# Optimization experiments

Measured on AMD Instinct MI355X. Metric: run time of the kernel, lower is better.

The kernel has to match this reference:

```python
import jax, jax.numpy as jnp
import numpy as np
import math

D = 2048      # hidden_size
H = 16        # num_heads
DH = 128      # head_dim
RQ = 1024     # q_rank
RK = 512      # kv_rank
B, T = 2, 2048

def setup_inputs() -> dict:
    key = jax.random.key(0)
    ks = jax.random.split(key, 8)
    s = lambda fan_in: 1.0 / math.sqrt(fan_in)
    return {
        "x": jax.random.normal(ks[0], (B, T, D), dtype=jnp.float32),
        "Wq_down": jax.random.normal(ks[1], (RQ, D), dtype=jnp.float32) * s(D),
        "Wkv_down": jax.random.normal(ks[2], (RK, D), dtype=jnp.float32) * s(D),
        "Wq_up": jax.random.normal(ks[3], (D, RQ), dtype=jnp.float32) * s(RQ),
        "Wk_up": jax.random.normal(ks[4], (D, RK), dtype=jnp.float32) * s(RK),
        "Wv_up": jax.random.normal(ks[5], (D, RK), dtype=jnp.float32) * s(RK),
        "Wo": jax.random.normal(ks[6], (D, D), dtype=jnp.float32) * s(D),
        "bo": jnp.zeros((D,), dtype=jnp.float32),
    }

def _heads_view(w, rank):
    # w: [H*DH, rank] -> [H, rank, DH]  (matches torch view(H,DH,r).transpose(1,2))
    return w.reshape(H, DH, rank).transpose(0, 2, 1)

def reference(x, Wq_down, Wkv_down, Wq_up, Wk_up, Wv_up, Wo, bo):
    Bx, Tx, d = x.shape
    # low-rank down-projections (torch Linear: x @ W.T)
    Q_lat = x @ Wq_down.T            # [B,T,RQ]
    C_kv = x @ Wkv_down.T            # [B,S,RK]  (S == T, no cache)
    S = C_kv.shape[1]
    # absorbed score matrix M = Uq Uk^T / sqrt(d_h): [H,RQ,RK]
    Uq_h = _heads_view(Wq_up, RQ)    # [H,RQ,DH]
    Uk_h = _heads_view(Wk_up, RK)    # [H,RK,DH]
    Mmat = jnp.einsum('hqd,hkd->hqk', Uq_h, Uk_h) * (1.0 / math.sqrt(DH))
    # logits in latent space: [B,H,T,S]
    logits = jnp.einsum('btq,hqk,bsk->bhts', Q_lat, Mmat, C_kv)
    # causal mask (P = S - T = 0)
    P = S - Tx
    i = jnp.arange(Tx)[:, None]
    j = jnp.arange(S)[None, :]
    neg_inf = jnp.float32(-jnp.inf)
    logits = jnp.where((j > P + i)[None, None], neg_inf, logits)
    # fp32 softmax (every causal row has >=1 valid key, no NaNs)
    attn = jax.nn.softmax(logits.astype(jnp.float32), axis=-1).astype(x.dtype)
    # value up-projection per head: [B,H,S,DH]
    Uv_h = _heads_view(Wv_up, RK)    # [H,RK,DH]
    V_up = jnp.einsum('bsr,hrd->bhsd', C_kv, Uv_h)
    ctx = jnp.einsum('bhts,bhsd->bhtd', attn, V_up)      # [B,H,T,DH]
    ctx = ctx.transpose(0, 2, 1, 3).reshape(Bx, Tx, H * DH)
    out = ctx @ Wo.T + bo
    return out
```

## Files before the change

kernel.cpp:

```cpp
#include <hip/hip_runtime.h>

typedef __bf16 bf16x8 __attribute__((ext_vector_type(8)));
typedef float f32x4 __attribute__((ext_vector_type(4)));
typedef float f32x16 __attribute__((ext_vector_type(16)));
typedef unsigned short u16x4 __attribute__((ext_vector_type(4)));
typedef unsigned int u32x4 __attribute__((ext_vector_type(4)));

#define L2E 1.44269504088896340736f

__device__ __forceinline__ f32x4 mfma16(bf16x8 a, bf16x8 b, f32x4 c) {
  return __builtin_amdgcn_mfma_f32_16x16x32_bf16(a, b, c, 0, 0, 0);
}
__device__ __forceinline__ f32x16 mfma32(bf16x8 a, bf16x8 b, f32x16 c) {
  return __builtin_amdgcn_mfma_f32_32x32x16_bf16(a, b, c, 0, 0, 0);
}

__device__ __forceinline__ void async16(const __bf16* g, __bf16* l) {
  __builtin_amdgcn_global_load_lds(
      (const __attribute__((address_space(1))) void*)g,
      (__attribute__((address_space(3))) void*)l, 16, 0, 0);
}

__device__ __forceinline__ unsigned pk(float x, float y) {
  unsigned short lo = __builtin_bit_cast(unsigned short, (__bf16)x);
  unsigned short hi = __builtin_bit_cast(unsigned short, (__bf16)y);
  return ((unsigned)hi << 16) | (unsigned)lo;
}

__global__ __launch_bounds__(256) void cvt_all(
    const float* __restrict__ x, const float* __restrict__ wqd,
    const float* __restrict__ wkvd, const float* __restrict__ wqup,
    const float* __restrict__ wkup, const float* __restrict__ wvup,
    __bf16* __restrict__ dx, __bf16* __restrict__ dqkv,
    __bf16* __restrict__ dqu, __bf16* __restrict__ dku,
    __bf16* __restrict__ dvu) {
  int bx = blockIdx.x;
  const float* s;
  __bf16* d;
  int off;
  if (bx < 8192)       { s = x;    d = dx;                off = bx; }
  else if (bx < 10240) { s = wqd;  d = dqkv;              off = bx - 8192; }
  else if (bx < 11264) { s = wkvd; d = dqkv + 1024 * 2048; off = bx - 10240; }
  else if (bx < 13312) { s = wqup; d = dqu;               off = bx - 11264; }
  else if (bx < 14336) { s = wkup; d = dku;               off = bx - 13312; }
  else                 { s = wvup; d = dvu;               off = bx - 14336; }
  long i = (long)off * 1024 + threadIdx.x * 4;
  f32x4 v = *(const f32x4*)(s + i);
  u16x4 o;
#pragma unroll
  for (int j = 0; j < 4; j++) o[j] = __builtin_bit_cast(unsigned short, (__bf16)v[j]);
  *(u16x4*)((unsigned short*)d + i) = o;
}

__global__ __launch_bounds__(256) void cvt_bf16(const float* __restrict__ s,
                                                __bf16* __restrict__ d) {
  long i = (long)(blockIdx.x * 256 + threadIdx.x) * 4;
  f32x4 v = *(const f32x4*)(s + i);
  u16x4 o;
#pragma unroll
  for (int j = 0; j < 4; j++) o[j] = __builtin_bit_cast(unsigned short, (__bf16)v[j]);
  *(u16x4*)((unsigned short*)d + i) = o;
}

template <int OUTF32>
__device__ __forceinline__ void gemm_body(
    __bf16* As, __bf16* Bs, const __bf16* __restrict__ A,
    const __bf16* __restrict__ Bt, void* __restrict__ Cout,
    const float* __restrict__ bias, int lda, int ldb, int ldc, int N, int K,
    float scale, int bx, int by, int permn) {
  const int tid = threadIdx.x;
  const int wid = tid >> 6, lane = tid & 63;
  const int lrow = lane & 15, lkhi = lane >> 4;
  const int row0 = bx * 128, col0 = by * 128;
  const int wr = (wid >> 1) * 64, wc = (wid & 1) * 64;

  const int trow = tid >> 2;
  const int scol = 8 * ((tid & 3) ^ (trow & 3));
  const __bf16* pA0 = A + (size_t)(row0 + trow) * lda + scol;
  const __bf16* pA1 = pA0 + (size_t)64 * lda;
  const __bf16* pB0 = Bt + (size_t)(col0 + trow) * ldb + scol;
  const __bf16* pB1 = pB0 + (size_t)64 * ldb;
  __bf16* lA0 = As + wid * 512;
  __bf16* lA1 = As + 2048 + wid * 512;
  __bf16* lB0 = Bs + wid * 512;
  __bf16* lB1 = Bs + 2048 + wid * 512;

  int aoff[4], boff[4];
#pragma unroll
  for (int i = 0; i < 4; i++) {
    int rr = wr + i * 16 + lrow;
    aoff[i] = rr * 32 + 8 * (lkhi ^ (rr & 3));
    rr = wc + i * 16 + lrow;
    boff[i] = rr * 32 + 8 * (lkhi ^ (rr & 3));
  }

  f32x4 acc[4][4] = {};
  for (int k0 = 0; k0 < K; k0 += 32) {
    __syncthreads();
    async16(pA0, lA0);
    async16(pA1, lA1);
    async16(pB0, lB0);
    async16(pB1, lB1);
    pA0 += 32; pA1 += 32; pB0 += 32; pB1 += 32;
    __syncthreads();
    bf16x8 af[4], bv[4];
#pragma unroll
    for (int mi = 0; mi < 4; mi++) af[mi] = *(const bf16x8*)(As + aoff[mi]);
#pragma unroll
    for (int ni = 0; ni < 4; ni++) bv[ni] = *(const bf16x8*)(Bs + boff[ni]);
#pragma unroll
    for (int mi = 0; mi < 4; mi++)
#pragma unroll
      for (int ni = 0; ni < 4; ni++)
        acc[mi][ni] = mfma16(af[mi], bv[ni], acc[mi][ni]);
  }

  const int orow = row0 + wr + lkhi * 4;
  const int prow = permn ? ((lrow & 3) | ((lrow & 4) << 1) | ((lrow & 8) >> 1))
                         : lrow;
  const int ocol = col0 + wc + prow;
#pragma unroll
  for (int mi = 0; mi < 4; mi++)
#pragma unroll
    for (int ni = 0; ni < 4; ni++)
#pragma unroll
      for (int r = 0; r < 4; r++) {
        size_t idx = (size_t)(orow + mi * 16 + r) * ldc + (ocol + ni * 16);
        float v = acc[mi][ni][r] * scale;
        if (OUTF32)
          ((float*)Cout)[idx] = v + bias[ocol + ni * 16];
        else
          ((__bf16*)Cout)[idx] = (__bf16)v;
      }
}

template <int OUTF32, int PERMN = 0>
__global__ __launch_bounds__(256, 3) void gemm_bt(
    const __bf16* __restrict__ A, const __bf16* __restrict__ Bt,
    void* __restrict__ Cout, const float* __restrict__ bias,
    int lda, int ldb, int ldc, int N, int K, float scale) {
  __shared__ __align__(16) __bf16 As[4096];
  __shared__ __align__(16) __bf16 Bs[4096];
  gemm_body<OUTF32>(As, Bs, A, Bt, Cout, bias, lda, ldb, ldc, N, K, scale,
                    blockIdx.x, blockIdx.y, PERMN);
}

__global__ __launch_bounds__(256, 3) void gemm_mid(
    const __bf16* __restrict__ qlat, const __bf16* __restrict__ ckv,
    const __bf16* __restrict__ wqu, const __bf16* __restrict__ wku,
    const __bf16* __restrict__ wvu, __bf16* __restrict__ qf,
    __bf16* __restrict__ kf, __bf16* __restrict__ vt) {
  __shared__ __align__(16) __bf16 As[4096];
  __shared__ __align__(16) __bf16 Bs[4096];
  int bid = (int)blockIdx.x;
  if (bid < 512) {
    gemm_body<0>(As, Bs, qlat, wqu, qf, nullptr, 1536, 1024, 2048, 2048, 1024,
                 0.12752039360437355f, bid & 31, bid >> 5, 0);
  } else if (bid < 1024) {
    bid -= 512;
    gemm_body<0>(As, Bs, ckv, wku, kf, nullptr, 1536, 512, 2048, 2048, 512,
                 1.0f, bid & 31, bid >> 5, 0);
  } else {
    bid -= 1024;
    gemm_body<0>(As, Bs, wvu, ckv, vt, nullptr, 512, 1536, 4096, 4096, 512,
                 1.0f, bid & 15, bid >> 4, 1);
  }
}

__global__ __launch_bounds__(512, 1) void mla_attn(
    const __bf16* __restrict__ Qf, const __bf16* __restrict__ Kf,
    const __bf16* __restrict__ Vt, __bf16* __restrict__ ctx) {
  __shared__ __align__(16) __bf16 SM[2][32768];
  __shared__ float MLm[128], MLl[128];

  const int bid = (int)blockIdx.x;
  const int qt = 15 - (bid >> 5);
  const int bh = bid & 31;
  const int h = bh >> 1, b = bh & 1;
  const int tid = threadIdx.x;
  const int half = tid >> 8;
  const int htid = tid & 255;
  const int wid4 = htid >> 6;
  const int lane = tid & 63;
  const int l31 = lane & 31;
  const bool hh = (lane & 32) != 0;

  __bf16* Ks = &SM[half][0];
  __bf16* Vs = &SM[half][16384];

  const __bf16* Kbh = Kf + (size_t)b * 2048 * 2048 + h * 128;
  const __bf16* Vbh = Vt + (size_t)h * 128 * 4096 + b * 2048;

  auto stage = [&](int k0, int buf) {
#pragma unroll
    for (int i = 0; i < 4; i++) {
      int e = i * 2048 + htid * 8;
      int krow = e >> 7;
      int kcol = (e & 127) ^ (8 * (krow & 15));
      async16(Kbh + (size_t)(k0 + krow) * 2048 + kcol,
              Ks + buf * 8192 + i * 2048 + wid4 * 512);
    }
#pragma unroll
    for (int i = 0; i < 4; i++) {
      int e = i * 2048 + htid * 8;
      int vrow = e >> 6;
      int vcol = (e & 63) ^ (8 * (vrow & 7));
      async16(Vbh + (size_t)vrow * 4096 + k0 + vcol,
              Vs + buf * 8192 + i * 2048 + wid4 * 512);
    }
  };

  const int q0 = qt * 128;
  const int ntile = qt + 1;
  const int kbase = half * ntile;
  const int q = q0 + wid4 * 32 + l31;

  bf16x8 qb[8];
  const __bf16* qrow =
      Qf + (size_t)(b * 2048 + q) * 2048 + h * 128 + (hh ? 8 : 0);
#pragma unroll
  for (int ds = 0; ds < 8; ds++) qb[ds] = *(const bf16x8*)(qrow + ds * 16);

  f32x16 o[4] = {};
  float mrow = 0.f, lsum = 0.f;

  int cur = 0;
  stage(kbase * 64, 0);

  for (int t = 0; t < ntile; t++) {
    const int kb = kbase + t;
    const int k0 = kb * 64;
    __syncthreads();
    if (t + 1 < ntile) stage(k0 + 64, cur ^ 1);

    f32x16 sa[2] = {}, sb[2] = {};
    __builtin_amdgcn_s_setprio(1);
#pragma unroll
    for (int ds = 0; ds < 4; ds++) {
#pragma unroll
      for (int kt = 0; kt < 2; kt++) {
        int row = kt * 32 + l31;
        int col = (ds * 16 + (hh ? 8 : 0)) ^ (8 * (row & 15));
        bf16x8 kfr = *(const bf16x8*)(Ks + cur * 8192 + row * 128 + col);
        sa[kt] = mfma32(kfr, qb[ds], sa[kt]);
      }
    }
#pragma unroll
    for (int ds = 4; ds < 8; ds++) {
#pragma unroll
      for (int kt = 0; kt < 2; kt++) {
        int row = kt * 32 + l31;
        int col = (ds * 16 + (hh ? 8 : 0)) ^ (8 * (row & 15));
        bf16x8 kfr = *(const bf16x8*)(Ks + cur * 8192 + row * 128 + col);
        sb[kt] = mfma32(kfr, qb[ds], sb[kt]);
      }
    }
    __builtin_amdgcn_s_setprio(0);
    f32x16 sacc[2];
    sacc[0] = sa[0] + sb[0];
    sacc[1] = sa[1] + sb[1];

    if (kb >= 2 * qt) {
#pragma unroll
      for (int kt = 0; kt < 2; kt++)
#pragma unroll
        for (int r = 0; r < 16; r++) {
          int key = k0 + kt * 32 + (r & 3) + 8 * (r >> 2) + (hh ? 4 : 0);
          if (key > q) sacc[kt][r] = -1e30f;
        }
    }

    float t16[16];
#pragma unroll
    for (int r = 0; r < 16; r++) t16[r] = fmaxf(sacc[0][r], sacc[1][r]);
#pragma unroll
    for (int s = 8; s; s >>= 1)
#pragma unroll
      for (int r = 0; r < s; r++) t16[r] = fmaxf(t16[r], t16[r + s]);
    float pm = fmaxf(t16[0], __shfl_xor(t16[0], 32));

    float ps0 = 0.f, ps1 = 0.f, ps2 = 0.f, ps3 = 0.f;
#pragma unroll
    for (int kt = 0; kt < 2; kt++)
#pragma unroll
      for (int r = 0; r < 16; r += 4) {
        float a0 = __builtin_amdgcn_exp2f(sacc[kt][r + 0] - mrow);
        float a1 = __builtin_amdgcn_exp2f(sacc[kt][r + 1] - mrow);
        float a2 = __builtin_amdgcn_exp2f(sacc[kt][r + 2] - mrow);
        float a3 = __builtin_amdgcn_exp2f(sacc[kt][r + 3] - mrow);
        sacc[kt][r + 0] = a0; sacc[kt][r + 1] = a1;
        sacc[kt][r + 2] = a2; sacc[kt][r + 3] = a3;
        ps0 += a0; ps1 += a1; ps2 += a2; ps3 += a3;
      }

    __builtin_amdgcn_s_setprio(1);
#pragma unroll
    for (int s = 0; s < 4; s++) {
      const int kt = s >> 1, r8 = (s & 1) * 8;
      u32x4 wv;
      wv.x = pk(sacc[kt][r8 + 0], sacc[kt][r8 + 1]);
      wv.y = pk(sacc[kt][r8 + 2], sacc[kt][r8 + 3]);
      wv.z = pk(sacc[kt][r8 + 4], sacc[kt][r8 + 5]);
      wv.w = pk(sacc[kt][r8 + 6], sacc[kt][r8 + 7]);
      bf16x8 pa = __builtin_bit_cast(bf16x8, wv);
#pragma unroll
      for (int dt = 0; dt < 4; dt++) {
        int vrow = dt * 32 + l31;
        int vcol = (s * 16 + (hh ? 8 : 0)) ^ (8 * (vrow & 7));
        bf16x8 vf = *(const bf16x8*)(Vs + cur * 8192 + vrow * 64 + vcol);
        o[dt] = mfma32(pa, vf, o[dt]);
      }
    }
    __builtin_amdgcn_s_setprio(0);

    float ps = (ps0 + ps1) + (ps2 + ps3);
    ps += __shfl_xor(ps, 32);
    lsum += ps;

    if (__any(pm > mrow + 8.f)) {
      float mn = fmaxf(mrow, pm);
      float sf = __builtin_amdgcn_exp2f(mrow - mn);
      mrow = mn;
      lsum *= sf;
#pragma unroll
      for (int r = 0; r < 16; r++) {
        int ql = (r & 3) + 8 * (r >> 2) + (hh ? 4 : 0);
        float sr = __shfl(sf, ql);
#pragma unroll
        for (int dt = 0; dt < 4; dt++) o[dt][r] *= sr;
      }
    }
    cur ^= 1;
  }

  __syncthreads();
  float* om = (float*)&SM[1][0];
  if (half == 1) {
#pragma unroll
    for (int dt = 0; dt < 4; dt++) {
      int base = ((wid4 * 4 + dt) * 64 + lane) * 16;
#pragma unroll
      for (int r = 0; r < 16; r++) om[base + r] = o[dt][r];
    }
    if (!hh) { MLm[wid4 * 32 + l31] = mrow; MLl[wid4 * 32 + l31] = lsum; }
  }
  __syncthreads();
  if (half == 0) {
#pragma unroll
    for (int r = 0; r < 16; r++) {
      int ql = (r & 3) + 8 * (r >> 2) + (hh ? 4 : 0);
      float m0r = __shfl(mrow, ql);
      float l0r = __shfl(lsum, ql);
      float m1r = MLm[wid4 * 32 + ql];
      float l1r = MLl[wid4 * 32 + ql];
      float M = fmaxf(m0r, m1r);
      float w0 = __builtin_amdgcn_exp2f(m0r - M);
      float w1 = __builtin_amdgcn_exp2f(m1r - M);
      float inv = 1.f / (l0r * w0 + l1r * w1);
      size_t rowi = (size_t)(b * 2048 + q0 + wid4 * 32 + ql) * 2048 + h * 128;
#pragma unroll
      for (int dt = 0; dt < 4; dt++) {
        float o1v = om[((wid4 * 4 + dt) * 64 + lane) * 16 + r];
        ctx[rowi + dt * 32 + l31] = (__bf16)((o[dt][r] * w0 + o1v * w1) * inv);
      }
    }
  }
}

extern "C" void kernel_launch(void* const* d_in, const int* in_sizes, int n_in,
                              void* d_out, int out_size, void* d_ws, size_t ws_size,
                              hipStream_t stream) {
  (void)in_sizes; (void)n_in; (void)out_size; (void)ws_size;
  const float* x    = (const float*)d_in[0];
  const float* wqd  = (const float*)d_in[1];
  const float* wkvd = (const float*)d_in[2];
  const float* wqup = (const float*)d_in[3];
  const float* wkup = (const float*)d_in[4];
  const float* wvup = (const float*)d_in[5];
  const float* wo   = (const float*)d_in[6];
  const float* bo   = (const float*)d_in[7];

  char* ws = (char*)d_ws;
  const size_t MB = 1024 * 1024;
  __bf16* x_bf     = (__bf16*)(ws + 0);
  __bf16* q_full   = (__bf16*)(ws + 16 * MB);
  __bf16* k_full   = (__bf16*)(ws + 32 * MB);
  __bf16* vt       = (__bf16*)(ws + 48 * MB);
  __bf16* qkv_lat  = (__bf16*)(ws + 64 * MB);
  __bf16* wqkvd_bf = (__bf16*)(ws + 76 * MB);
  __bf16* wqup_bf  = (__bf16*)(ws + 82 * MB);
  __bf16* wkup_bf  = (__bf16*)(ws + 86 * MB);
  __bf16* wvup_bf  = (__bf16*)(ws + 88 * MB);
  __bf16* ctx   = x_bf;
  __bf16* wo_bf = qkv_lat;

  cvt_all<<<15360, 256, 0, stream>>>(x, wqd, wkvd, wqup, wkup, wvup, x_bf,
                                     wqkvd_bf, wqup_bf, wkup_bf, wvup_bf);

  dim3 blk(256);
  gemm_bt<0><<<dim3(32, 12), blk, 0, stream>>>(x_bf, wqkvd_bf, qkv_lat, nullptr,
                                               2048, 2048, 1536, 1536, 2048, 1.0f);
  gemm_mid<<<1536, blk, 0, stream>>>(qkv_lat, qkv_lat + 1024, wqup_bf, wkup_bf,
                                     wvup_bf, q_full, k_full, vt);
  cvt_bf16<<<4096, 256, 0, stream>>>(wo, wo_bf);
  mla_attn<<<512, 512, 0, stream>>>(q_full, k_full, vt, ctx);
  gemm_bt<1><<<dim3(32, 16), blk, 0, stream>>>(ctx, wo_bf, (float*)d_out, bo,
                                               2048, 2048, 2048, 2048, 2048, 1.0f);
}
```

Baseline: 217.7 us.

## Software-pipeline QK^T of next tile with softmax and PV of current tile

Splits K and V staging into separate async loads and issues K two tiles ahead and V one tile ahead. The QK^T MFMAs for tile t+1 run in the same iteration as the softmax and PV of tile t, so matrix-core work overlaps the exp/reduction VALU work. Synchronisation moves to one barrier at the end of each iteration. It holds an extra set of score accumulators live, which raises register pressure and may lower occupancy.

```diff
diff --git a/kernel.cpp b/kernel.cpp
--- a/kernel.cpp
+++ b/kernel.cpp
@@ -191,7 +191,7 @@
   const __bf16* Kbh = Kf + (size_t)b * 2048 * 2048 + h * 128;
   const __bf16* Vbh = Vt + (size_t)h * 128 * 4096 + b * 2048;
 
-  auto stage = [&](int k0, int buf) {
+  auto stageK = [&](int k0, int buf) {
 #pragma unroll
     for (int i = 0; i < 4; i++) {
       int e = i * 2048 + htid * 8;
@@ -200,6 +200,8 @@
       async16(Kbh + (size_t)(k0 + krow) * 2048 + kcol,
               Ks + buf * 8192 + i * 2048 + wid4 * 512);
     }
+  };
+  auto stageV = [&](int k0, int buf) {
 #pragma unroll
     for (int i = 0; i < 4; i++) {
       int e = i * 2048 + htid * 8;
@@ -221,44 +223,55 @@
 #pragma unroll
   for (int ds = 0; ds < 8; ds++) qb[ds] = *(const bf16x8*)(qrow + ds * 16);
 
+  auto computeQK = [&](int buf, f32x16* s) {
+    f32x16 sa0 = {}, sa1 = {}, sb0 = {}, sb1 = {};
+    const __bf16* kp = Ks + buf * 8192;
+    __builtin_amdgcn_s_setprio(1);
+#pragma unroll
+    for (int ds = 0; ds < 4; ds++) {
+      int row0_ = l31, row1_ = 32 + l31;
+      int c0 = (ds * 16 + (hh ? 8 : 0)) ^ (8 * (row0_ & 15));
+      int c1 = (ds * 16 + (hh ? 8 : 0)) ^ (8 * (row1_ & 15));
+      bf16x8 k0f = *(const bf16x8*)(kp + row0_ * 128 + c0);
+      bf16x8 k1f = *(const bf16x8*)(kp + row1_ * 128 + c1);
+      sa0 = mfma32(k0f, qb[ds], sa0);
+      sa1 = mfma32(k1f, qb[ds], sa1);
+    }
+#pragma unroll
+    for (int ds = 4; ds < 8; ds++) {
+      int row0_ = l31, row1_ = 32 + l31;
+      int c0 = (ds * 16 + (hh ? 8 : 0)) ^ (8 * (row0_ & 15));
+      int c1 = (ds * 16 + (hh ? 8 : 0)) ^ (8 * (row1_ & 15));
+      bf16x8 k0f = *(const bf16x8*)(kp + row0_ * 128 + c0);
+      bf16x8 k1f = *(const bf16x8*)(kp + row1_ * 128 + c1);
+      sb0 = mfma32(k0f, qb[ds], sb0);
+      sb1 = mfma32(k1f, qb[ds], sb1);
+    }
+    __builtin_amdgcn_s_setprio(0);
+    s[0] = sa0 + sb0;
+    s[1] = sa1 + sb1;
+  };
+
   f32x16 o[4] = {};
   float mrow = 0.f, lsum = 0.f;
 
-  int cur = 0;
-  stage(kbase * 64, 0);
+  stageK(kbase * 64, 0);
+  stageV(kbase * 64, 0);
+  if (ntile > 1) stageK(kbase * 64 + 64, 1);
+  __syncthreads();
+  f32x16 scur[2];
+  computeQK(0, scur);
+  __syncthreads();
 
   for (int t = 0; t < ntile; t++) {
     const int kb = kbase + t;
     const int k0 = kb * 64;
-    __syncthreads();
-    if (t + 1 < ntile) stage(k0 + 64, cur ^ 1);
-
-    f32x16 sa[2] = {}, sb[2] = {};
-    __builtin_amdgcn_s_setprio(1);
-#pragma unroll
-    for (int ds = 0; ds < 4; ds++) {
-#pragma unroll
-      for (int kt = 0; kt < 2; kt++) {
-        int row = kt * 32 + l31;
-        int col = (ds * 16 + (hh ? 8 : 0)) ^ (8 * (row & 15));
-        bf16x8 kfr = *(const bf16x8*)(Ks + cur * 8192 + row * 128 + col);
-        sa[kt] = mfma32(kfr, qb[ds], sa[kt]);
-      }
-    }
-#pragma unroll
-    for (int ds = 4; ds < 8; ds++) {
-#pragma unroll
-      for (int kt = 0; kt < 2; kt++) {
-        int row = kt * 32 + l31;
-        int col = (ds * 16 + (hh ? 8 : 0)) ^ (8 * (row & 15));
-        bf16x8 kfr = *(const bf16x8*)(Ks + cur * 8192 + row * 128 + col);
-        sb[kt] = mfma32(kfr, qb[ds], sb[kt]);
-      }
-    }
-    __builtin_amdgcn_s_setprio(0);
-    f32x16 sacc[2];
-    sacc[0] = sa[0] + sb[0];
-    sacc[1] = sa[1] + sb[1];
+
+    if (t + 2 < ntile) stageK(k0 + 128, t & 1);
+    if (t + 1 < ntile) stageV(k0 + 64, (t + 1) & 1);
+
+    f32x16 snext[2];
+    if (t + 1 < ntile) computeQK((t + 1) & 1, snext);
 
     if (kb >= 2 * qt) {
 #pragma unroll
@@ -266,13 +279,13 @@
 #pragma unroll
         for (int r = 0; r < 16; r++) {
           int key = k0 + kt * 32 + (r & 3) + 8 * (r >> 2) + (hh ? 4 : 0);
-          if (key > q) sacc[kt][r] = -1e30f;
+          if (key > q) scur[kt][r] = -1e30f;
         }
     }
 
     float t16[16];
 #pragma unroll
-    for (int r = 0; r < 16; r++) t16[r] = fmaxf(sacc[0][r], sacc[1][r]);
+    for (int r = 0; r < 16; r++) t16[r] = fmaxf(scur[0][r], scur[1][r]);
 #pragma unroll
     for (int s = 8; s; s >>= 1)
 #pragma unroll
@@ -284,12 +297,12 @@
     for (int kt = 0; kt < 2; kt++)
 #pragma unroll
       for (int r = 0; r < 16; r += 4) {
-        float a0 = __builtin_amdgcn_exp2f(sacc[kt][r + 0] - mrow);
-        float a1 = __builtin_amdgcn_exp2f(sacc[kt][r + 1] - mrow);
-        float a2 = __builtin_amdgcn_exp2f(sacc[kt][r + 2] - mrow);
-        float a3 = __builtin_amdgcn_exp2f(sacc[kt][r + 3] - mrow);
-        sacc[kt][r + 0] = a0; sacc[kt][r + 1] = a1;
-        sacc[kt][r + 2] = a2; sacc[kt][r + 3] = a3;
+        float a0 = __builtin_amdgcn_exp2f(scur[kt][r + 0] - mrow);
+        float a1 = __builtin_amdgcn_exp2f(scur[kt][r + 1] - mrow);
+        float a2 = __builtin_amdgcn_exp2f(scur[kt][r + 2] - mrow);
+        float a3 = __builtin_amdgcn_exp2f(scur[kt][r + 3] - mrow);
+        scur[kt][r + 0] = a0; scur[kt][r + 1] = a1;
+        scur[kt][r + 2] = a2; scur[kt][r + 3] = a3;
         ps0 += a0; ps1 += a1; ps2 += a2; ps3 += a3;
       }
 
@@ -298,16 +311,16 @@
     for (int s = 0; s < 4; s++) {
       const int kt = s >> 1, r8 = (s & 1) * 8;
       u32x4 wv;
-      wv.x = pk(sacc[kt][r8 + 0], sacc[kt][r8 + 1]);
-      wv.y = pk(sacc[kt][r8 + 2], sacc[kt][r8 + 3]);
-      wv.z = pk(sacc[kt][r8 + 4], sacc[kt][r8 + 5]);
-      wv.w = pk(sacc[kt][r8 + 6], sacc[kt][r8 + 7]);
+      wv.x = pk(scur[kt][r8 + 0], scur[kt][r8 + 1]);
+      wv.y = pk(scur[kt][r8 + 2], scur[kt][r8 + 3]);
+      wv.z = pk(scur[kt][r8 + 4], scur[kt][r8 + 5]);
+      wv.w = pk(scur[kt][r8 + 6], scur[kt][r8 + 7]);
       bf16x8 pa = __builtin_bit_cast(bf16x8, wv);
 #pragma unroll
       for (int dt = 0; dt < 4; dt++) {
         int vrow = dt * 32 + l31;
         int vcol = (s * 16 + (hh ? 8 : 0)) ^ (8 * (vrow & 7));
-        bf16x8 vf = *(const bf16x8*)(Vs + cur * 8192 + vrow * 64 + vcol);
+        bf16x8 vf = *(const bf16x8*)(Vs + (t & 1) * 8192 + vrow * 64 + vcol);
         o[dt] = mfma32(pa, vf, o[dt]);
       }
     }
@@ -330,10 +343,11 @@
         for (int dt = 0; dt < 4; dt++) o[dt][r] *= sr;
       }
     }
-    cur ^= 1;
-  }
-
-  __syncthreads();
+
+    __syncthreads();
+    if (t + 1 < ntile) { scur[0] = snext[0]; scur[1] = snext[1]; }
+  }
+
   float* om = (float*)&SM[1][0];
   if (half == 1) {
 #pragma unroll
```

Result: slower. 251.3 us (+15.4%).
